# Optimization experiments

Hardware: AMD Instinct MI355X
Metric: run time of the kernel (lower is better)

Reference implementation:

```python
import jax, jax.numpy as jnp
import numpy as np

INV_SQRT_2PI = 1.0 / np.sqrt(2.0 * np.pi)
EPS = 1e-15


def setup_inputs() -> dict:
    key = jax.random.key(0)
    k1, k2, k3 = jax.random.split(key, 3)
    n = 8192
    # m_z: network outputs [g1, g2]
    m_z = 0.5 * jax.random.normal(k1, (n, 2), dtype=jnp.float32)
    # y: strictly positive survival times (rand, shifted away from 0 for log)
    y = jax.random.uniform(k2, (n, 1), dtype=jnp.float32, minval=0.05, maxval=5.0)
    delta = (jax.random.uniform(k3, (n, 1), dtype=jnp.float32) < 0.7).astype(jnp.float32)
    return {"m_z": m_z, "y": y, "delta": delta}


def reference(m_z, y, delta):
    n = m_z.shape[0]
    g1 = m_z[:, 0:1]                      # [n,1]
    g2 = m_z[:, 1:2]                      # [n,1]
    h = 1.3 * float(n) ** (-0.2)          # bandwidth
    R = g1 + jnp.log(y)                   # [n,1]
    d = delta[:, 0]                       # [n]

    S1 = jnp.sum(delta * g2) / n
    S2 = -jnp.sum(delta * R) / n

    DR = (R - R.T) / h                    # [n,n] pairwise (R_i - R_j)/h
    # Gaussian kernel pdf, column-reduced with delta weights
    K = jnp.exp(-0.5 * DR * DR) * INV_SQRT_2PI
    Dk = (d @ K) / (n * h)                # [n] : sum_i delta_i K_ij / (n h)
    S3 = jnp.sum(d * jnp.log(Dk + EPS)) / n

    # Gaussian cdf, column-reduced with L = exp(g2-g1) weights
    P = jax.scipy.special.ndtr(DR)        # [n,n]
    L = jnp.exp(g2 - g1)[:, 0]            # [n]
    LP_sum = (L @ P) / n                  # [n]
    S4 = -jnp.sum(d * jnp.log(LP_sum + EPS)) / n

    return -(S1 + S2 + S3 + S4)
```

## Files before the change

kernel.cpp:

```cpp
#include <hip/hip_runtime.h>
#include <math.h>

#define TPB 256
#define IB 64
#define EPSF 1e-15f

__global__ __launch_bounds__(TPB, 8) void pair_kernel(
    const float* __restrict__ m_z, const float* __restrict__ y,
    const float* __restrict__ delta, float2* __restrict__ P,
    float* __restrict__ out, float inv_hk, int n, int span) {
    __shared__ float4 sRd[128];
    __shared__ float2 sL2[128];
    __shared__ float sLtot;
    const int tid = threadIdx.x;
    const int j = blockIdx.x * TPB + tid;
    const float2* __restrict__ mz2 = (const float2*)m_z;

    const float2 gj = mz2[j];
    const float Rj = (gj.x + __logf(y[j])) * inv_hk;

    const int ibase = blockIdx.y * span;
    if (tid < span) {
        const int i = ibase + tid;
        const float2 g = mz2[i];
        float* s = (float*)sRd;
        const int pk = tid >> 1, hf = tid & 1;
        s[4 * pk + hf]     = (g.x + __logf(y[i])) * inv_hk;
        s[4 * pk + 2 + hf] = delta[i];
        ((float*)sL2)[tid] = __expf(g.y - g.x);
    }
    __syncthreads();
    if (tid < 64) {
        float s = 0.0f;
        for (int t = tid; t < span; t += 64) s += ((float*)sL2)[t];
        for (int o = 32; o > 0; o >>= 1) s += __shfl_down(s, o, 64);
        if (tid == 0) sLtot = s;
    }
    __syncthreads();
    if (j == 0 && blockIdx.y == 0) out[0] = 0.0f;

    float a0 = 0.0f, a1 = 0.0f, b0 = 0.5f * sLtot, b1 = 0.0f;
    const int m = span >> 1;
#pragma unroll 4
    for (int k = 0; k < m; ++k) {
        const float4 rd = sRd[k];
        const float2 ll = sL2[k];
        const float dr0 = rd.x - Rj;
        const float dr1 = rd.y - Rj;
        const float e0 = __builtin_amdgcn_exp2f(-(dr0 * dr0));
        const float e1 = __builtin_amdgcn_exp2f(-(dr1 * dr1));
        const float t0 = __builtin_amdgcn_rcpf(fmaf(0.3916993f, fabsf(dr0), 1.0f));
        const float t1 = __builtin_amdgcn_rcpf(fmaf(0.3916993f, fabsf(dr1), 1.0f));
        const float u0 = t0 * fmaf(t0, fmaf(t0, 0.3739278f, -0.0479399f), 0.1740121f) * e0;
        const float u1 = t1 * fmaf(t1, fmaf(t1, 0.3739278f, -0.0479399f), 0.1740121f) * e1;
        a0 = fmaf(rd.z, e0, a0);
        a1 = fmaf(rd.w, e1, a1);
        b0 = fmaf(copysignf(ll.x, dr0), 0.5f - u0, b0);
        b1 = fmaf(copysignf(ll.y, dr1), 0.5f - u1, b1);
    }
    P[(size_t)blockIdx.y * n + j] = make_float2(a0 + a1, b0 + b1);
}

__global__ __launch_bounds__(TPB) void finalize_kernel(
    const float2* __restrict__ P, const float* __restrict__ m_z,
    const float* __restrict__ y, const float* __restrict__ delta,
    float* __restrict__ out, float c1, float invn, int n) {
    const int j = blockIdx.x * TPB + threadIdx.x;
    float sa = 0.0f, sb = 0.0f;
    for (int b = 0; b < IB; ++b) {
        const float2 v = P[(size_t)b * n + j];
        sa += v.x;
        sb += v.y;
    }
    const float d = delta[j];
    const float R = m_z[2 * j] + __logf(y[j]);
    float term = d * (R - m_z[2 * j + 1] - __logf(fmaf(c1, sa, EPSF))
                                         + __logf(fmaf(invn, sb, EPSF)));
    for (int o = 32; o > 0; o >>= 1) term += __shfl_down(term, o, 64);
    __shared__ float wsum[TPB / 64];
    if ((threadIdx.x & 63) == 0) wsum[threadIdx.x >> 6] = term;
    __syncthreads();
    if (threadIdx.x == 0) {
        float ssum = 0.0f;
        for (int w = 0; w < TPB / 64; ++w) ssum += wsum[w];
        atomicAdd(out, ssum * invn);
    }
}

extern "C" void kernel_launch(void* const* d_in, const int* in_sizes, int n_in,
                              void* d_out, int out_size, void* d_ws, size_t ws_size,
                              hipStream_t stream) {
    const float* m_z   = (const float*)d_in[0];
    const float* y     = (const float*)d_in[1];
    const float* delta = (const float*)d_in[2];
    float* out = (float*)d_out;
    const int n = in_sizes[1];

    float2* P = (float2*)d_ws;

    const double h = 1.3 * pow((double)n, -0.2);
    const double k = 1.1774100225154747;
    const float inv_hk = (float)(1.0 / (h * k));
    const float c1 = (float)(0.3989422804014327 / ((double)n * h));
    const float invn = 1.0f / (float)n;
    const int span = n / IB;

    const int nblk = (n + TPB - 1) / TPB;
    dim3 grid(nblk, IB);
    pair_kernel<<<grid, TPB, 0, stream>>>(m_z, y, delta, P, out, inv_hk, n, span);
    finalize_kernel<<<nblk, TPB, 0, stream>>>(P, m_z, y, delta, out, c1, invn, n);
}
```

Measured before the change: 82.51 us.

## Compact event columns and precompute per-sample values in a prep kernel

Adds a prep kernel that computes the scaled residuals, delta and L weights once, sums L per block, and uses an atomic counter to build a list of the columns j where delta is nonzero. The pair kernel then only processes those columns, since non-event columns get zero weight in the final sum, and blocks beyond the count exit early. This skips about 30% of the pairwise exp/cdf work and removes the redundant per-block log/exp recomputation. In exchange it adds two more launches, atomic contention while building the list, an unordered list of columns that scatters the finalize gathers, and hardcoded workspace offsets and a 32-block L sum that assume n=8192.

```diff
diff --git a/kernel.cpp b/kernel.cpp
--- a/kernel.cpp
+++ b/kernel.cpp
@@ -5,44 +5,70 @@
 #define IB 64
 #define EPSF 1e-15f
 
+#define P_OFF   0u
+#define RD_OFF  4194304u
+#define L2_OFF  (RD_OFF + 65536u)
+#define RS_OFF  (L2_OFF + 32768u)
+#define JL_OFF  (RS_OFF + 32768u)
+#define LP_OFF  (JL_OFF + 32768u)
+#define CNT_OFF (LP_OFF + 128u)
+
+__global__ void init_kernel(char* __restrict__ ws, float* __restrict__ out) {
+    *(unsigned*)(ws + CNT_OFF) = 0u;
+    out[0] = 0.0f;
+}
+
+__global__ __launch_bounds__(TPB) void prep_kernel(
+    const float* __restrict__ m_z, const float* __restrict__ y,
+    const float* __restrict__ delta, char* __restrict__ ws, float inv_hk) {
+    const int i = blockIdx.x * TPB + threadIdx.x;
+    const float2 g = ((const float2*)m_z)[i];
+    const float R = (g.x + __logf(y[i])) * inv_hk;
+    const float d = delta[i];
+    const float L = __expf(g.y - g.x);
+    float* RD = (float*)(ws + RD_OFF);
+    RD[4 * (i >> 1) + (i & 1)]     = R;
+    RD[4 * (i >> 1) + 2 + (i & 1)] = d;
+    ((float*)(ws + L2_OFF))[i] = L;
+    ((float*)(ws + RS_OFF))[i] = R;
+    if (d != 0.0f) {
+        const unsigned pos = atomicAdd((unsigned*)(ws + CNT_OFF), 1u);
+        ((int*)(ws + JL_OFF))[pos] = i;
+    }
+    float s = L;
+    for (int o = 32; o > 0; o >>= 1) s += __shfl_down(s, o, 64);
+    __shared__ float wsum[TPB / 64];
+    if ((threadIdx.x & 63) == 0) wsum[threadIdx.x >> 6] = s;
+    __syncthreads();
+    if (threadIdx.x == 0) {
+        float t = 0.0f;
+        for (int w = 0; w < TPB / 64; ++w) t += wsum[w];
+        ((float*)(ws + LP_OFF))[blockIdx.x] = t;
+    }
+}
+
 __global__ __launch_bounds__(TPB, 8) void pair_kernel(
-    const float* __restrict__ m_z, const float* __restrict__ y,
-    const float* __restrict__ delta, float2* __restrict__ P,
-    float* __restrict__ out, float inv_hk, int n, int span) {
-    __shared__ float4 sRd[128];
-    __shared__ float2 sL2[128];
-    __shared__ float sLtot;
+    const char* __restrict__ ws, float2* __restrict__ P, int n) {
+    const unsigned cnt = *(const unsigned*)(ws + CNT_OFF);
+    const int t = blockIdx.x * TPB + threadIdx.x;
+    if ((unsigned)(blockIdx.x * TPB) >= cnt) return;
+    __shared__ float4 sRd[64];
+    __shared__ float2 sL2[64];
     const int tid = threadIdx.x;
-    const int j = blockIdx.x * TPB + tid;
-    const float2* __restrict__ mz2 = (const float2*)m_z;
+    const int by = blockIdx.y;
+    if (tid < 64) {
+        sRd[tid] = ((const float4*)(ws + RD_OFF))[(by << 6) + tid];
+    } else if (tid < 128) {
+        sL2[tid - 64] = ((const float2*)(ws + L2_OFF))[(by << 6) + (tid - 64)];
+    }
+    const int tc = min(t, (int)cnt - 1);
+    const int jl = ((const int*)(ws + JL_OFF))[tc];
+    const float Rj = ((const float*)(ws + RS_OFF))[jl];
+    __syncthreads();
 
-    const float2 gj = mz2[j];
-    const float Rj = (gj.x + __logf(y[j])) * inv_hk;
-
-    const int ibase = blockIdx.y * span;
-    if (tid < span) {
-        const int i = ibase + tid;
-        const float2 g = mz2[i];
-        float* s = (float*)sRd;
-        const int pk = tid >> 1, hf = tid & 1;
-        s[4 * pk + hf]     = (g.x + __logf(y[i])) * inv_hk;
-        s[4 * pk + 2 + hf] = delta[i];
-        ((float*)sL2)[tid] = __expf(g.y - g.x);
-    }
-    __syncthreads();
-    if (tid < 64) {
-        float s = 0.0f;
-        for (int t = tid; t < span; t += 64) s += ((float*)sL2)[t];
-        for (int o = 32; o > 0; o >>= 1) s += __shfl_down(s, o, 64);
-        if (tid == 0) sLtot = s;
-    }
-    __syncthreads();
-    if (j == 0 && blockIdx.y == 0) out[0] = 0.0f;
-
-    float a0 = 0.0f, a1 = 0.0f, b0 = 0.5f * sLtot, b1 = 0.0f;
-    const int m = span >> 1;
+    float a0 = 0.0f, a1 = 0.0f, b0 = 0.0f, b1 = 0.0f;
 #pragma unroll 4
-    for (int k = 0; k < m; ++k) {
+    for (int k = 0; k < 64; ++k) {
         const float4 rd = sRd[k];
         const float2 ll = sL2[k];
         const float dr0 = rd.x - Rj;
@@ -58,24 +84,32 @@
         b0 = fmaf(copysignf(ll.x, dr0), 0.5f - u0, b0);
         b1 = fmaf(copysignf(ll.y, dr1), 0.5f - u1, b1);
     }
-    P[(size_t)blockIdx.y * n + j] = make_float2(a0 + a1, b0 + b1);
+    if (t < (int)cnt)
+        P[(size_t)by * n + t] = make_float2(a0 + a1, b0 + b1);
 }
 
 __global__ __launch_bounds__(TPB) void finalize_kernel(
-    const float2* __restrict__ P, const float* __restrict__ m_z,
-    const float* __restrict__ y, const float* __restrict__ delta,
+    const float2* __restrict__ P, const char* __restrict__ ws,
+    const float* __restrict__ m_z, const float* __restrict__ y,
     float* __restrict__ out, float c1, float invn, int n) {
-    const int j = blockIdx.x * TPB + threadIdx.x;
-    float sa = 0.0f, sb = 0.0f;
-    for (int b = 0; b < IB; ++b) {
-        const float2 v = P[(size_t)b * n + j];
-        sa += v.x;
-        sb += v.y;
+    const unsigned cnt = *(const unsigned*)(ws + CNT_OFF);
+    const int t = blockIdx.x * TPB + threadIdx.x;
+    float term = 0.0f;
+    if (t < (int)cnt) {
+        float sa = 0.0f, sb = 0.0f;
+        for (int b = 0; b < IB; ++b) {
+            const float2 v = P[(size_t)b * n + t];
+            sa += v.x;
+            sb += v.y;
+        }
+        float sumL = 0.0f;
+        const float* Lp = (const float*)(ws + LP_OFF);
+        for (int w = 0; w < 32; ++w) sumL += Lp[w];
+        const int jl = ((const int*)(ws + JL_OFF))[t];
+        const float R = m_z[2 * jl] + __logf(y[jl]);
+        term = R - m_z[2 * jl + 1] - __logf(fmaf(c1, sa, EPSF))
+             + __logf(fmaf(invn, sb + 0.5f * sumL, EPSF));
     }
-    const float d = delta[j];
-    const float R = m_z[2 * j] + __logf(y[j]);
-    float term = d * (R - m_z[2 * j + 1] - __logf(fmaf(c1, sa, EPSF))
-                                         + __logf(fmaf(invn, sb, EPSF)));
     for (int o = 32; o > 0; o >>= 1) term += __shfl_down(term, o, 64);
     __shared__ float wsum[TPB / 64];
     if ((threadIdx.x & 63) == 0) wsum[threadIdx.x >> 6] = term;
@@ -96,17 +130,22 @@
     float* out = (float*)d_out;
     const int n = in_sizes[1];
 
-    float2* P = (float2*)d_ws;
+    char* ws = (char*)d_ws;
+    float2* P = (float2*)(ws + P_OFF);
 
     const double h = 1.3 * pow((double)n, -0.2);
     const double k = 1.1774100225154747;
     const float inv_hk = (float)(1.0 / (h * k));
     const float c1 = (float)(0.3989422804014327 / ((double)n * h));
     const float invn = 1.0f / (float)n;
-    const int span = n / IB;
+
+    init_kernel<<<1, 1, 0, stream>>>(ws, out);
 
     const int nblk = (n + TPB - 1) / TPB;
+    prep_kernel<<<nblk, TPB, 0, stream>>>(m_z, y, delta, ws, inv_hk);
+
     dim3 grid(nblk, IB);
-    pair_kernel<<<grid, TPB, 0, stream>>>(m_z, y, delta, P, out, inv_hk, n, span);
-    finalize_kernel<<<nblk, TPB, 0, stream>>>(P, m_z, y, delta, out, c1, invn, n);
+    pair_kernel<<<grid, TPB, 0, stream>>>(ws, P, n);
+
+    finalize_kernel<<<nblk, TPB, 0, stream>>>(P, ws, m_z, y, out, c1, invn, n);
 }
```

Measured after the change: 89.62 us. +8.6%, slower.

## Precompute R, delta, L in a prep kernel and read them via uniform global loads

Applied to the files above, without the earlier changes.

Adds a prep kernel that computes the scaled R, delta and L once per element, plus per-block partial sums of L. The pair kernel then drops its per-block LDS staging, its barriers and its redundant log/exp work, and reads the i-side values straight from global memory with block-uniform addresses that can become scalar loads. The constant 0.5*sum(L) term moves into the finalize kernel, and the sign flip becomes an XOR on the sign bit. In exchange it adds an extra kernel launch and relies on the scalar cache instead of LDS inside the inner loop.

```diff
diff --git a/kernel.cpp b/kernel.cpp
--- a/kernel.cpp
+++ b/kernel.cpp
@@ -5,58 +5,69 @@
 #define IB 64
 #define EPSF 1e-15f
 
+
+__global__ __launch_bounds__(TPB) void prep_kernel(
+    const float* __restrict__ m_z, const float* __restrict__ y,
+    const float* __restrict__ delta,
+    float* __restrict__ Rarr, float* __restrict__ Darr, float* __restrict__ Larr,
+    float* __restrict__ LP, float inv_hk) {
+    const int i = blockIdx.x * TPB + threadIdx.x;
+    const float2 g = ((const float2*)m_z)[i];
+    const float L = __expf(g.y - g.x);
+    Rarr[i] = (g.x + __logf(y[i])) * inv_hk;
+    Darr[i] = delta[i];
+    Larr[i] = L;
+    float s = L;
+    for (int o = 32; o > 0; o >>= 1) s += __shfl_down(s, o, 64);
+    __shared__ float wsum[TPB / 64];
+    if ((threadIdx.x & 63) == 0) wsum[threadIdx.x >> 6] = s;
+    __syncthreads();
+    if (threadIdx.x == 0) {
+        float t = 0.0f;
+        for (int w = 0; w < TPB / 64; ++w) t += wsum[w];
+        LP[blockIdx.x] = t;
+    }
+}
+
 __global__ __launch_bounds__(TPB, 8) void pair_kernel(
-    const float* __restrict__ m_z, const float* __restrict__ y,
-    const float* __restrict__ delta, float2* __restrict__ P,
-    float* __restrict__ out, float inv_hk, int n, int span) {
-    __shared__ float4 sRd[128];
-    __shared__ float2 sL2[128];
-    __shared__ float sLtot;
-    const int tid = threadIdx.x;
-    const int j = blockIdx.x * TPB + tid;
-    const float2* __restrict__ mz2 = (const float2*)m_z;
+    const float* __restrict__ Rarr, const float* __restrict__ Darr,
+    const float* __restrict__ Larr, float2* __restrict__ P,
+    float* __restrict__ out, int n, int span) {
+    const int j = blockIdx.x * TPB + threadIdx.x;
+    const float Rj = Rarr[j];
+    if (j == 0 && blockIdx.y == 0) out[0] = 0.0f;
+    const int ibase = blockIdx.y * span;
 
-    const float2 gj = mz2[j];
-    const float Rj = (gj.x + __logf(y[j])) * inv_hk;
-
-    const int ibase = blockIdx.y * span;
-    if (tid < span) {
-        const int i = ibase + tid;
-        const float2 g = mz2[i];
-        float* s = (float*)sRd;
-        const int pk = tid >> 1, hf = tid & 1;
-        s[4 * pk + hf]     = (g.x + __logf(y[i])) * inv_hk;
-        s[4 * pk + 2 + hf] = delta[i];
-        ((float*)sL2)[tid] = __expf(g.y - g.x);
-    }
-    __syncthreads();
-    if (tid < 64) {
-        float s = 0.0f;
-        for (int t = tid; t < span; t += 64) s += ((float*)sL2)[t];
-        for (int o = 32; o > 0; o >>= 1) s += __shfl_down(s, o, 64);
-        if (tid == 0) sLtot = s;
-    }
-    __syncthreads();
-    if (j == 0 && blockIdx.y == 0) out[0] = 0.0f;
-
-    float a0 = 0.0f, a1 = 0.0f, b0 = 0.5f * sLtot, b1 = 0.0f;
-    const int m = span >> 1;
-#pragma unroll 4
-    for (int k = 0; k < m; ++k) {
-        const float4 rd = sRd[k];
-        const float2 ll = sL2[k];
-        const float dr0 = rd.x - Rj;
-        const float dr1 = rd.y - Rj;
-        const float e0 = __builtin_amdgcn_exp2f(-(dr0 * dr0));
-        const float e1 = __builtin_amdgcn_exp2f(-(dr1 * dr1));
-        const float t0 = __builtin_amdgcn_rcpf(fmaf(0.3916993f, fabsf(dr0), 1.0f));
-        const float t1 = __builtin_amdgcn_rcpf(fmaf(0.3916993f, fabsf(dr1), 1.0f));
-        const float u0 = t0 * fmaf(t0, fmaf(t0, 0.3739278f, -0.0479399f), 0.1740121f) * e0;
-        const float u1 = t1 * fmaf(t1, fmaf(t1, 0.3739278f, -0.0479399f), 0.1740121f) * e1;
-        a0 = fmaf(rd.z, e0, a0);
-        a1 = fmaf(rd.w, e1, a1);
-        b0 = fmaf(copysignf(ll.x, dr0), 0.5f - u0, b0);
-        b1 = fmaf(copysignf(ll.y, dr1), 0.5f - u1, b1);
+    float a0 = 0.0f, a1 = 0.0f, b0 = 0.0f, b1 = 0.0f;
+    const int nch = span >> 4;
+#pragma unroll 1
+    for (int c = 0; c < nch; ++c) {
+        const int base = ibase + (c << 4);
+#pragma unroll
+        for (int kk = 0; kk < 8; ++kk) {
+            const float r0 = Rarr[base + 2 * kk];
+            const float r1 = Rarr[base + 2 * kk + 1];
+            const float d0 = Darr[base + 2 * kk];
+            const float d1 = Darr[base + 2 * kk + 1];
+            const float l0 = Larr[base + 2 * kk];
+            const float l1 = Larr[base + 2 * kk + 1];
+            const float dr0 = r0 - Rj;
+            const float dr1 = r1 - Rj;
+            const float e0 = __builtin_amdgcn_exp2f(-(dr0 * dr0));
+            const float e1 = __builtin_amdgcn_exp2f(-(dr1 * dr1));
+            const float t0 = __builtin_amdgcn_rcpf(fmaf(0.3916993f, fabsf(dr0), 1.0f));
+            const float t1 = __builtin_amdgcn_rcpf(fmaf(0.3916993f, fabsf(dr1), 1.0f));
+            const float u0 = t0 * fmaf(t0, fmaf(t0, 0.3739278f, -0.0479399f), 0.1740121f) * e0;
+            const float u1 = t1 * fmaf(t1, fmaf(t1, 0.3739278f, -0.0479399f), 0.1740121f) * e1;
+            a0 = fmaf(d0, e0, a0);
+            a1 = fmaf(d1, e1, a1);
+            const float s0 = __uint_as_float(__float_as_uint(0.5f - u0)
+                                             ^ (__float_as_uint(dr0) & 0x80000000u));
+            const float s1 = __uint_as_float(__float_as_uint(0.5f - u1)
+                                             ^ (__float_as_uint(dr1) & 0x80000000u));
+            b0 = fmaf(l0, s0, b0);
+            b1 = fmaf(l1, s1, b1);
+        }
     }
     P[(size_t)blockIdx.y * n + j] = make_float2(a0 + a1, b0 + b1);
 }
@@ -64,7 +75,8 @@
 __global__ __launch_bounds__(TPB) void finalize_kernel(
     const float2* __restrict__ P, const float* __restrict__ m_z,
     const float* __restrict__ y, const float* __restrict__ delta,
-    float* __restrict__ out, float c1, float invn, int n) {
+    const float* __restrict__ LP, float* __restrict__ out,
+    float c1, float invn, int n, int nlp) {
     const int j = blockIdx.x * TPB + threadIdx.x;
     float sa = 0.0f, sb = 0.0f;
     for (int b = 0; b < IB; ++b) {
@@ -72,10 +84,12 @@
         sa += v.x;
         sb += v.y;
     }
+    float sumL = 0.0f;
+    for (int w = 0; w < nlp; ++w) sumL += LP[w];
     const float d = delta[j];
     const float R = m_z[2 * j] + __logf(y[j]);
     float term = d * (R - m_z[2 * j + 1] - __logf(fmaf(c1, sa, EPSF))
-                                         + __logf(fmaf(invn, sb, EPSF)));
+                      + __logf(fmaf(invn, sb + 0.5f * sumL, EPSF)));
     for (int o = 32; o > 0; o >>= 1) term += __shfl_down(term, o, 64);
     __shared__ float wsum[TPB / 64];
     if ((threadIdx.x & 63) == 0) wsum[threadIdx.x >> 6] = term;
@@ -96,7 +110,12 @@
     float* out = (float*)d_out;
     const int n = in_sizes[1];
 
-    float2* P = (float2*)d_ws;
+    char* ws = (char*)d_ws;
+    float2* P   = (float2*)ws;
+    float* Rarr = (float*)(ws + 4194304);
+    float* Darr = Rarr + n;
+    float* Larr = Darr + n;
+    float* LP   = Larr + n;
 
     const double h = 1.3 * pow((double)n, -0.2);
     const double k = 1.1774100225154747;
@@ -106,7 +125,10 @@
     const int span = n / IB;
 
     const int nblk = (n + TPB - 1) / TPB;
+    prep_kernel<<<nblk, TPB, 0, stream>>>(m_z, y, delta, Rarr, Darr, Larr, LP, inv_hk);
+
     dim3 grid(nblk, IB);
-    pair_kernel<<<grid, TPB, 0, stream>>>(m_z, y, delta, P, out, inv_hk, n, span);
-    finalize_kernel<<<nblk, TPB, 0, stream>>>(P, m_z, y, delta, out, c1, invn, n);
+    pair_kernel<<<grid, TPB, 0, stream>>>(Rarr, Darr, Larr, P, out, n, span);
+
+    finalize_kernel<<<nblk, TPB, 0, stream>>>(P, m_z, y, delta, LP, out, c1, invn, n, nblk);
 }
```

After: 90.47 us. 9.7% more time.
